# Kernel optimization log

Hardware: AMD Instinct MI355X
Metric: run time of the kernel (lower is better)

Reference implementation:

```python
import jax, jax.numpy as jnp
import numpy as np

B, N, H = 16, 1024, 768
NEG_INF = -9e15
SLOPE = 0.2


def setup_inputs() -> dict:
    key = jax.random.key(0)
    k1, k2, k3, k4, k5 = jax.random.split(key, 5)
    x = jax.random.normal(k1, (B, N, H), dtype=jnp.float32)
    # node_length acts as a per-node validity mask (float, used via outer product)
    lengths = jax.random.randint(k2, (B,), N // 2, N)
    node_length = (jnp.arange(N)[None, :] < lengths[:, None]).astype(jnp.float32)
    # sparse-ish binary adjacency with self-loops
    adj = (jax.random.uniform(k3, (B, N, N)) < 0.05).astype(jnp.float32)
    adj = jnp.maximum(adj, jnp.eye(N, dtype=jnp.float32)[None])
    # params: kaiming-normal init
    W = jax.random.normal(k4, (H, H), dtype=jnp.float32) * np.sqrt(2.0 / H)
    a = jax.random.normal(k5, (2 * H, 1), dtype=jnp.float32) * np.sqrt(2.0 / (2 * H))
    return {"input": x, "node_length": node_length, "graph_structure": adj, "W": W, "a": a}


def reference(input, node_length, graph_structure, W, a):
    # node_vec = A @ X  [B,N,H]
    node_vec = jnp.matmul(graph_structure, input)
    h = jnp.matmul(node_vec, W)  # [B,N,F]
    F_ = W.shape[1]
    a1 = a[:F_, 0]   # weights on h_i
    a2 = a[F_:, 0]   # weights on h_j
    # e[b,i,j] = leaky_relu(h_i . a1 + h_j . a2)  (identical to concat+matmul with a)
    s1 = jnp.einsum("bnf,f->bn", h, a1)
    s2 = jnp.einsum("bnf,f->bn", h, a2)
    e = jax.nn.leaky_relu(s1[:, :, None] + s2[:, None, :], negative_slope=SLOPE)
    # bias = outer product of node_length; mask where adj or bias <= 1e-6
    bias = node_length[:, :, None] * node_length[:, None, :]
    valid = (graph_structure > 1e-6) & (bias > 1e-6)
    scores = jnp.where(valid, e, NEG_INF)
    attn = jax.nn.softmax(scores, axis=-1)  # attn_dropout=0 -> identity
    return node_vec, attn
```

## Files before the change

kernel.cpp:

```cpp
#include <hip/hip_runtime.h>
#include <hip/hip_bf16.h>

#define BB 16
#define NN 1024
#define HH 768
#define NEG_INF_ -9.0e15f
#define SLOPE_ 0.2f

typedef __bf16 bh8 __attribute__((ext_vector_type(8)));
typedef __bf16 bh4 __attribute__((ext_vector_type(4)));
typedef float f4 __attribute__((ext_vector_type(4)));
typedef unsigned int u32;
typedef unsigned long long u64;


__device__ __forceinline__ float wave_sum0(float v) {
    #pragma unroll
    for (int off = 32; off > 0; off >>= 1) v += __shfl_down(v, off, 64);
    return v;
}
__device__ __forceinline__ float wave_sum_all(float v) {
    #pragma unroll
    for (int off = 1; off < 64; off <<= 1) v += __shfl_xor(v, off, 64);
    return v;
}
__device__ __forceinline__ float wave_max_all(float v) {
    #pragma unroll
    for (int off = 1; off < 64; off <<= 1) v = fmaxf(v, __shfl_xor(v, off, 64));
    return v;
}


__device__ __forceinline__ void gl_lds16(const void* g, void* l) {
    __builtin_amdgcn_global_load_lds(
        (const __attribute__((address_space(1))) u32*)g,
        (__attribute__((address_space(3))) u32*)l, 16, 0, 0);
}


__global__ __launch_bounds__(256) void prep_kernel(const float* __restrict__ adj,
                                                   const float* __restrict__ W,
                                                   const float* __restrict__ a,
                                                   u64* __restrict__ bits,
                                                   float* __restrict__ wa1,
                                                   float* __restrict__ wa2,
                                                   float* __restrict__ s1,
                                                   float* __restrict__ s2) {
    const int bid = blockIdx.x;
    const int tid = threadIdx.x;
    const int wave = tid >> 6, lane = tid & 63;

    const int gid = bid * 256 + tid;
    if (gid < BB * NN) { s1[gid] = 0.f; s2[gid] = 0.f; }

    const int row = bid * 4 + wave;
    const float* ar = adj + (size_t)row * NN;
    const int seg = lane >> 4;
    const int sh = (lane & 15) * 4;
    #pragma unroll
    for (int i = 0; i < 4; i++) {
        const int j = lane * 4 + i * 256;
        const float4 av = *(const float4*)(ar + j);
        u32 nib = (av.x > 1e-6f ? 1u : 0u) | (av.y > 1e-6f ? 2u : 0u)
                | (av.z > 1e-6f ? 4u : 0u) | (av.w > 1e-6f ? 8u : 0u);
        u64 word = (u64)nib << sh;
        word |= __shfl_xor(word, 8, 16);
        word |= __shfl_xor(word, 4, 16);
        word |= __shfl_xor(word, 2, 16);
        word |= __shfl_xor(word, 1, 16);
        if ((lane & 15) == 0) bits[(size_t)row * 16 + i * 4 + seg] = word;
    }

    if (bid < 192) {
        const int f = bid * 4 + wave;
        const float* Wr = W + (size_t)f * HH;
        float v1 = 0.f, v2 = 0.f;
        #pragma unroll
        for (int i = 0; i < 3; i++) {
            const int h = lane * 4 + i * 256;
            const float4 w  = *(const float4*)(Wr + h);
            const float4 a1 = *(const float4*)(a + h);
            const float4 a2 = *(const float4*)(a + HH + h);
            v1 += w.x * a1.x + w.y * a1.y + w.z * a1.z + w.w * a1.w;
            v2 += w.x * a2.x + w.y * a2.y + w.z * a2.z + w.w * a2.w;
        }
        v1 = wave_sum0(v1);
        v2 = wave_sum0(v2);
        if (lane == 0) { wa1[f] = v1; wa2[f] = v2; }
    }
}


__global__ __launch_bounds__(256) void xt_kernel(const float* __restrict__ x,
                                                 __bf16* __restrict__ xT) {
    __shared__ __bf16 T[32][36];
    const int b = blockIdx.z, nt = blockIdx.y, ht = blockIdx.x;
    const int t = threadIdx.x;
    const int r = t >> 3;
    const int c = (t & 7) * 4;
    const float4 v = *(const float4*)(x + ((size_t)b * NN + nt * 32 + r) * HH + ht * 32 + c);
    T[r][c + 0] = (__bf16)v.x; T[r][c + 1] = (__bf16)v.y;
    T[r][c + 2] = (__bf16)v.z; T[r][c + 3] = (__bf16)v.w;

    __syncthreads();
    const int h = t >> 3;
    const int nc = (t & 7) * 4;
    bh4 o = { T[nc + 0][h], T[nc + 1][h], T[nc + 2][h], T[nc + 3][h] };
    *(bh4*)(xT + ((size_t)b * HH + ht * 32 + h) * NN + nt * 32 + nc) = o;
}


#define BW 17

__global__ __launch_bounds__(256) void gemm_bits(const u64* __restrict__ bits,
                                                 const __bf16* __restrict__ xT,
                                                 const float* __restrict__ wa1,
                                                 const float* __restrict__ wa2,
                                                 float* __restrict__ out,
                                                 float* __restrict__ s1,
                                                 float* __restrict__ s2) {
    __shared__ __bf16 LUT[256 * 8];
    __shared__ u64 bitsL[128 * BW];
    __shared__ __bf16 Bs[128 * 64];
    const int b = blockIdx.z, bm = blockIdx.y, bn = blockIdx.x;
    const int tid = threadIdx.x, lane = tid & 63, wave = tid >> 6;
    const int wr = (wave >> 1) << 6;
    const int wc = (wave & 1) << 6;
    const int quad = lane >> 4, l16 = lane & 15;

    {
        bh8 e;
        #pragma unroll
        for (int j = 0; j < 8; j++) e[j] = ((tid >> j) & 1) ? (__bf16)1.0f : (__bf16)0.0f;
        *(bh8*)&LUT[tid * 8] = e;
    }
    {
        const u64* bg = bits + ((size_t)b * NN + bm * 128) * 16;
        #pragma unroll
        for (int q = 0; q < 8; q++) {
            const int g = tid * 8 + q;
            bitsL[(g >> 4) * BW + (g & 15)] = bg[g];
        }
    }

    const __bf16* Xb = xT + ((size_t)b * HH + bn * 128) * NN;

    f4 acc[4][4];
    #pragma unroll
    for (int i = 0; i < 4; i++)
        #pragma unroll
        for (int j = 0; j < 4; j++)
            acc[i][j] = (f4){0.f, 0.f, 0.f, 0.f};

    __syncthreads();

    for (int kt = 0; kt < NN; kt += 64) {
        #pragma unroll
        for (int it = 0; it < 4; it++) {
            const int c = tid + 256 * it;
            const int r = c >> 3, j = c & 7, kc = j ^ (r & 7);
            gl_lds16(Xb + (size_t)r * NN + kt + kc * 8, &Bs[r * 64 + j * 8]);
        }
        __syncthreads();

        const int w = kt >> 6;
        u64 aw[4];
        #pragma unroll
        for (int i = 0; i < 4; i++)
            aw[i] = bitsL[(wr + i * 16 + l16) * BW + w];

        #pragma unroll
        for (int s = 0; s < 2; s++) {
            bh8 af[4], bf_[4];
            #pragma unroll
            for (int i = 0; i < 4; i++) {
                const u32 byte = (u32)(aw[i] >> ((s * 4 + quad) * 8)) & 0xffu;
                af[i] = *(const bh8*)&LUT[byte * 8];
            }
            #pragma unroll
            for (int j = 0; j < 4; j++) {
                const int row = wc + j * 16 + l16;
                const int jj = (s * 4 + quad) ^ (row & 7);
                bf_[j] = *(const bh8*)&Bs[row * 64 + jj * 8];
            }
            #pragma unroll
            for (int i = 0; i < 4; i++)
                #pragma unroll
                for (int j = 0; j < 4; j++)
                    acc[i][j] = __builtin_amdgcn_mfma_f32_16x16x32_bf16(af[i], bf_[j], acc[i][j], 0, 0, 0);
        }
        __syncthreads();
    }

    float* Cb = out + (size_t)b * NN * HH + (size_t)bm * 128 * HH + bn * 128;
    const int rbase = wr + quad * 4;
    const int cbase = wc + l16;
    #pragma unroll
    for (int i = 0; i < 4; i++)
        #pragma unroll
        for (int j = 0; j < 4; j++)
            #pragma unroll
            for (int r = 0; r < 4; r++)
                Cb[(size_t)(rbase + i * 16 + r) * HH + cbase + j * 16] = acc[i][j][r];

    float w1j[4], w2j[4];
    #pragma unroll
    for (int j = 0; j < 4; j++) {
        w1j[j] = wa1[bn * 128 + cbase + j * 16];
        w2j[j] = wa2[bn * 128 + cbase + j * 16];
    }
    #pragma unroll
    for (int i = 0; i < 4; i++)
        #pragma unroll
        for (int r = 0; r < 4; r++) {
            float p1 = acc[i][0][r] * w1j[0] + acc[i][1][r] * w1j[1]
                     + acc[i][2][r] * w1j[2] + acc[i][3][r] * w1j[3];
            float p2 = acc[i][0][r] * w2j[0] + acc[i][1][r] * w2j[1]
                     + acc[i][2][r] * w2j[2] + acc[i][3][r] * w2j[3];
            p1 += __shfl_down(p1, 8, 16); p1 += __shfl_down(p1, 4, 16);
            p1 += __shfl_down(p1, 2, 16); p1 += __shfl_down(p1, 1, 16);
            p2 += __shfl_down(p2, 8, 16); p2 += __shfl_down(p2, 4, 16);
            p2 += __shfl_down(p2, 2, 16); p2 += __shfl_down(p2, 1, 16);
            if (l16 == 0) {
                const int n = b * NN + bm * 128 + rbase + i * 16 + r;
                atomicAdd(&s1[n], p1);
                atomicAdd(&s2[n], p2);
            }
        }
}


__global__ __launch_bounds__(256) void softmax_kernel(const u64* __restrict__ bits,
                                                      const float* __restrict__ nl,
                                                      const float* __restrict__ s1,
                                                      const float* __restrict__ s2,
                                                      float* __restrict__ attn) {
    const int row = blockIdx.x * 4 + (threadIdx.x >> 6);
    const int lane = threadIdx.x & 63;
    const int b = row >> 10, n = row & (NN - 1);
    const u64* bwr = bits + (size_t)row * 16;
    const float* nlb = nl + (size_t)b * NN;
    const float* s2b = s2 + (size_t)b * NN;
    const float s1v = s1[row];
    const bool rowok = nlb[n] > 1e-6f;
    const int bitbase = (lane & 15) * 4;

    f4 sc[4];
    float mx = NEG_INF_;
    #pragma unroll
    for (int i = 0; i < 4; i++) {
        const int j = lane * 4 + i * 256;
        const float4 sv = *(const float4*)(s2b + j);
        const float4 nv = *(const float4*)(nlb + j);
        const u64 w64 = bwr[i * 4 + (lane >> 4)];
        const float zs[4] = { s1v + sv.x, s1v + sv.y, s1v + sv.z, s1v + sv.w };
        const float ns[4] = { nv.x, nv.y, nv.z, nv.w };
        #pragma unroll
        for (int e = 0; e < 4; e++) {
            const float z = zs[e];
            const float lr = z > 0.f ? z : SLOPE_ * z;
            const bool valid = rowok && ((w64 >> (bitbase + e)) & 1ull) && (ns[e] > 1e-6f);
            sc[i][e] = valid ? lr : NEG_INF_;
            mx = fmaxf(mx, sc[i][e]);
        }
    }
    mx = wave_max_all(mx);

    f4 ex[4];
    float sum = 0.f;
    #pragma unroll
    for (int i = 0; i < 4; i++)
        #pragma unroll
        for (int e = 0; e < 4; e++) {
            ex[i][e] = __expf(sc[i][e] - mx);
            sum += ex[i][e];
        }
    sum = wave_sum_all(sum);
    const float inv = 1.0f / sum;

    float* outr = attn + (size_t)row * NN;
    #pragma unroll
    for (int i = 0; i < 4; i++) {
        const int j = lane * 4 + i * 256;
        float4 o;
        o.x = ex[i][0] * inv; o.y = ex[i][1] * inv;
        o.z = ex[i][2] * inv; o.w = ex[i][3] * inv;
        *(float4*)(outr + j) = o;
    }
}


extern "C" void kernel_launch(void* const* d_in, const int* in_sizes, int n_in,
                              void* d_out, int out_size, void* d_ws, size_t ws_size,
                              hipStream_t stream) {
    const float* x   = (const float*)d_in[0];
    const float* nl  = (const float*)d_in[1];
    const float* adj = (const float*)d_in[2];
    const float* W   = (const float*)d_in[3];
    const float* a   = (const float*)d_in[4];

    float* out = (float*)d_out;
    float* node_vec = out;
    float* attn = out + (size_t)BB * NN * HH;

    char* wsb = (char*)d_ws;
    float* wa1 = (float*)(wsb);
    float* wa2 = wa1 + HH;
    float* s1  = wa2 + HH;
    float* s2  = s1 + BB * NN;
    u64*    bits = (u64*)(wsb + (1u << 20));
    __bf16* xT   = (__bf16*)(wsb + (4u << 20));

    hipLaunchKernelGGL(prep_kernel, dim3(4096), dim3(256), 0, stream, adj, W, a, bits, wa1, wa2, s1, s2);
    hipLaunchKernelGGL(xt_kernel, dim3(24, 32, BB), dim3(256), 0, stream, x, xT);
    hipLaunchKernelGGL(gemm_bits, dim3(6, 8, BB), dim3(256), 0, stream, bits, xT, wa1, wa2, node_vec, s1, s2);
    hipLaunchKernelGGL(softmax_kernel, dim3(4096), dim3(256), 0, stream, bits, nl, s1, s2, attn);
}
```

Before: 275.2 us.

## Merge prep and transpose kernels, replace bitmask LUT A-tiles with dense bf16 adjacency

The adjacency prep and x-transpose kernels are merged into one launch using a split block index. The prep step now also writes a dense bf16 copy of the adjacency matrix. The GEMM streams that copy into LDS with async global-to-LDS loads, replacing the bitmask plus lookup-table decode of A fragments. This drops one launch and the LUT/bitmask LDS reads, but adds a 32 MB bf16 adjacency write in prep and 32 MB extra reads per GEMM pass instead of compact bits.

```diff
diff --git a/kernel.cpp b/kernel.cpp
--- a/kernel.cpp
+++ b/kernel.cpp
@@ -38,89 +38,92 @@
 }
 
 
-__global__ __launch_bounds__(256) void prep_kernel(const float* __restrict__ adj,
-                                                   const float* __restrict__ W,
-                                                   const float* __restrict__ a,
-                                                   u64* __restrict__ bits,
-                                                   float* __restrict__ wa1,
-                                                   float* __restrict__ wa2,
-                                                   float* __restrict__ s1,
-                                                   float* __restrict__ s2) {
+__global__ __launch_bounds__(256) void prep_xt_kernel(const float* __restrict__ adj,
+                                                      const float* __restrict__ W,
+                                                      const float* __restrict__ a,
+                                                      const float* __restrict__ x,
+                                                      u64* __restrict__ bits,
+                                                      __bf16* __restrict__ adjb,
+                                                      __bf16* __restrict__ xT,
+                                                      float* __restrict__ wa1,
+                                                      float* __restrict__ wa2,
+                                                      float* __restrict__ s1,
+                                                      float* __restrict__ s2) {
+    __shared__ __bf16 T[32][36];
     const int bid = blockIdx.x;
     const int tid = threadIdx.x;
     const int wave = tid >> 6, lane = tid & 63;
 
-    const int gid = bid * 256 + tid;
-    if (gid < BB * NN) { s1[gid] = 0.f; s2[gid] = 0.f; }
-
-    const int row = bid * 4 + wave;
-    const float* ar = adj + (size_t)row * NN;
-    const int seg = lane >> 4;
-    const int sh = (lane & 15) * 4;
-    #pragma unroll
-    for (int i = 0; i < 4; i++) {
-        const int j = lane * 4 + i * 256;
-        const float4 av = *(const float4*)(ar + j);
-        u32 nib = (av.x > 1e-6f ? 1u : 0u) | (av.y > 1e-6f ? 2u : 0u)
-                | (av.z > 1e-6f ? 4u : 0u) | (av.w > 1e-6f ? 8u : 0u);
-        u64 word = (u64)nib << sh;
-        word |= __shfl_xor(word, 8, 16);
-        word |= __shfl_xor(word, 4, 16);
-        word |= __shfl_xor(word, 2, 16);
-        word |= __shfl_xor(word, 1, 16);
-        if ((lane & 15) == 0) bits[(size_t)row * 16 + i * 4 + seg] = word;
-    }
-
-    if (bid < 192) {
-        const int f = bid * 4 + wave;
-        const float* Wr = W + (size_t)f * HH;
-        float v1 = 0.f, v2 = 0.f;
-        #pragma unroll
-        for (int i = 0; i < 3; i++) {
-            const int h = lane * 4 + i * 256;
-            const float4 w  = *(const float4*)(Wr + h);
-            const float4 a1 = *(const float4*)(a + h);
-            const float4 a2 = *(const float4*)(a + HH + h);
-            v1 += w.x * a1.x + w.y * a1.y + w.z * a1.z + w.w * a1.w;
-            v2 += w.x * a2.x + w.y * a2.y + w.z * a2.z + w.w * a2.w;
-        }
-        v1 = wave_sum0(v1);
-        v2 = wave_sum0(v2);
-        if (lane == 0) { wa1[f] = v1; wa2[f] = v2; }
-    }
-}
-
-
-__global__ __launch_bounds__(256) void xt_kernel(const float* __restrict__ x,
-                                                 __bf16* __restrict__ xT) {
-    __shared__ __bf16 T[32][36];
-    const int b = blockIdx.z, nt = blockIdx.y, ht = blockIdx.x;
-    const int t = threadIdx.x;
-    const int r = t >> 3;
-    const int c = (t & 7) * 4;
-    const float4 v = *(const float4*)(x + ((size_t)b * NN + nt * 32 + r) * HH + ht * 32 + c);
-    T[r][c + 0] = (__bf16)v.x; T[r][c + 1] = (__bf16)v.y;
-    T[r][c + 2] = (__bf16)v.z; T[r][c + 3] = (__bf16)v.w;
-
-    __syncthreads();
-    const int h = t >> 3;
-    const int nc = (t & 7) * 4;
-    bh4 o = { T[nc + 0][h], T[nc + 1][h], T[nc + 2][h], T[nc + 3][h] };
-    *(bh4*)(xT + ((size_t)b * HH + ht * 32 + h) * NN + nt * 32 + nc) = o;
-}
-
-
-#define BW 17
-
-__global__ __launch_bounds__(256) void gemm_bits(const u64* __restrict__ bits,
-                                                 const __bf16* __restrict__ xT,
-                                                 const float* __restrict__ wa1,
-                                                 const float* __restrict__ wa2,
-                                                 float* __restrict__ out,
-                                                 float* __restrict__ s1,
-                                                 float* __restrict__ s2) {
-    __shared__ __bf16 LUT[256 * 8];
-    __shared__ u64 bitsL[128 * BW];
+    if (bid < 4096) {
+        const int gid = bid * 256 + tid;
+        if (gid < BB * NN) { s1[gid] = 0.f; s2[gid] = 0.f; }
+
+        const int row = bid * 4 + wave;
+        const float* ar = adj + (size_t)row * NN;
+        __bf16* abr = adjb + (size_t)row * NN;
+        const int seg = lane >> 4;
+        const int sh = (lane & 15) * 4;
+        #pragma unroll
+        for (int i = 0; i < 4; i++) {
+            const int j = lane * 4 + i * 256;
+            const float4 av = *(const float4*)(ar + j);
+            bh4 o = { (__bf16)av.x, (__bf16)av.y, (__bf16)av.z, (__bf16)av.w };
+            *(bh4*)(abr + j) = o;
+            u32 nib = (av.x > 1e-6f ? 1u : 0u) | (av.y > 1e-6f ? 2u : 0u)
+                    | (av.z > 1e-6f ? 4u : 0u) | (av.w > 1e-6f ? 8u : 0u);
+            u64 word = (u64)nib << sh;
+            word |= __shfl_xor(word, 8, 16);
+            word |= __shfl_xor(word, 4, 16);
+            word |= __shfl_xor(word, 2, 16);
+            word |= __shfl_xor(word, 1, 16);
+            if ((lane & 15) == 0) bits[(size_t)row * 16 + i * 4 + seg] = word;
+        }
+
+        if (bid < 192) {
+            const int f = bid * 4 + wave;
+            const float* Wr = W + (size_t)f * HH;
+            float v1 = 0.f, v2 = 0.f;
+            #pragma unroll
+            for (int i = 0; i < 3; i++) {
+                const int h = lane * 4 + i * 256;
+                const float4 w  = *(const float4*)(Wr + h);
+                const float4 a1 = *(const float4*)(a + h);
+                const float4 a2 = *(const float4*)(a + HH + h);
+                v1 += w.x * a1.x + w.y * a1.y + w.z * a1.z + w.w * a1.w;
+                v2 += w.x * a2.x + w.y * a2.y + w.z * a2.z + w.w * a2.w;
+            }
+            v1 = wave_sum0(v1);
+            v2 = wave_sum0(v2);
+            if (lane == 0) { wa1[f] = v1; wa2[f] = v2; }
+        }
+    } else {
+        const int u = bid - 4096;
+        const int ht = u % 24;
+        const int nt = (u / 24) & 31;
+        const int b  = u / (24 * 32);
+        const int r = tid >> 3;
+        const int c = (tid & 7) * 4;
+        const float4 v = *(const float4*)(x + ((size_t)b * NN + nt * 32 + r) * HH + ht * 32 + c);
+        T[r][c + 0] = (__bf16)v.x; T[r][c + 1] = (__bf16)v.y;
+        T[r][c + 2] = (__bf16)v.z; T[r][c + 3] = (__bf16)v.w;
+
+        __syncthreads();
+        const int h = tid >> 3;
+        const int nc = (tid & 7) * 4;
+        bh4 o = { T[nc + 0][h], T[nc + 1][h], T[nc + 2][h], T[nc + 3][h] };
+        *(bh4*)(xT + ((size_t)b * HH + ht * 32 + h) * NN + nt * 32 + nc) = o;
+    }
+}
+
+
+__global__ __launch_bounds__(256) void gemm_dense(const __bf16* __restrict__ adjb,
+                                                  const __bf16* __restrict__ xT,
+                                                  const float* __restrict__ wa1,
+                                                  const float* __restrict__ wa2,
+                                                  float* __restrict__ out,
+                                                  float* __restrict__ s1,
+                                                  float* __restrict__ s2) {
+    __shared__ __bf16 As[128 * 64];
     __shared__ __bf16 Bs[128 * 64];
     const int b = blockIdx.z, bm = blockIdx.y, bn = blockIdx.x;
     const int tid = threadIdx.x, lane = tid & 63, wave = tid >> 6;
@@ -128,22 +131,18 @@
     const int wc = (wave & 1) << 6;
     const int quad = lane >> 4, l16 = lane & 15;
 
-    {
-        bh8 e;
-        #pragma unroll
-        for (int j = 0; j < 8; j++) e[j] = ((tid >> j) & 1) ? (__bf16)1.0f : (__bf16)0.0f;
-        *(bh8*)&LUT[tid * 8] = e;
-    }
-    {
-        const u64* bg = bits + ((size_t)b * NN + bm * 128) * 16;
-        #pragma unroll
-        for (int q = 0; q < 8; q++) {
-            const int g = tid * 8 + q;
-            bitsL[(g >> 4) * BW + (g & 15)] = bg[g];
-        }
-    }
-
-    const __bf16* Xb = xT + ((size_t)b * HH + bn * 128) * NN;
+    const __bf16* Ab = adjb + ((size_t)b * NN + bm * 128) * NN;
+    const __bf16* Xb = xT   + ((size_t)b * HH + bn * 128) * NN;
+
+    const __bf16* aSrc[4]; const __bf16* bSrc[4]; int dOff[4];
+    #pragma unroll
+    for (int it = 0; it < 4; it++) {
+        const int c = tid + 256 * it;
+        const int r = c >> 3, j = c & 7, kc = j ^ (r & 7);
+        aSrc[it] = Ab + (size_t)r * NN + kc * 8;
+        bSrc[it] = Xb + (size_t)r * NN + kc * 8;
+        dOff[it] = c * 8;
+    }
 
     f4 acc[4][4];
     #pragma unroll
@@ -152,30 +151,22 @@
         for (int j = 0; j < 4; j++)
             acc[i][j] = (f4){0.f, 0.f, 0.f, 0.f};
 
-    __syncthreads();
-
     for (int kt = 0; kt < NN; kt += 64) {
         #pragma unroll
         for (int it = 0; it < 4; it++) {
-            const int c = tid + 256 * it;
-            const int r = c >> 3, j = c & 7, kc = j ^ (r & 7);
-            gl_lds16(Xb + (size_t)r * NN + kt + kc * 8, &Bs[r * 64 + j * 8]);
+            gl_lds16(aSrc[it] + kt, &As[dOff[it]]);
+            gl_lds16(bSrc[it] + kt, &Bs[dOff[it]]);
         }
         __syncthreads();
-
-        const int w = kt >> 6;
-        u64 aw[4];
-        #pragma unroll
-        for (int i = 0; i < 4; i++)
-            aw[i] = bitsL[(wr + i * 16 + l16) * BW + w];
 
         #pragma unroll
         for (int s = 0; s < 2; s++) {
             bh8 af[4], bf_[4];
             #pragma unroll
             for (int i = 0; i < 4; i++) {
-                const u32 byte = (u32)(aw[i] >> ((s * 4 + quad) * 8)) & 0xffu;
-                af[i] = *(const bh8*)&LUT[byte * 8];
+                const int row = wr + i * 16 + l16;
+                const int jj = (s * 4 + quad) ^ (row & 7);
+                af[i] = *(const bh8*)&As[row * 64 + jj * 8];
             }
             #pragma unroll
             for (int j = 0; j < 4; j++) {
@@ -310,9 +301,11 @@
     float* s2  = s1 + BB * NN;
     u64*    bits = (u64*)(wsb + (1u << 20));
     __bf16* xT   = (__bf16*)(wsb + (4u << 20));
-
-    hipLaunchKernelGGL(prep_kernel, dim3(4096), dim3(256), 0, stream, adj, W, a, bits, wa1, wa2, s1, s2);
-    hipLaunchKernelGGL(xt_kernel, dim3(24, 32, BB), dim3(256), 0, stream, x, xT);
-    hipLaunchKernelGGL(gemm_bits, dim3(6, 8, BB), dim3(256), 0, stream, bits, xT, wa1, wa2, node_vec, s1, s2);
+    __bf16* adjb = (__bf16*)(wsb + (32u << 20));
+
+    hipLaunchKernelGGL(prep_xt_kernel, dim3(4096 + 24 * 32 * BB), dim3(256), 0, stream,
+                       adj, W, a, x, bits, adjb, xT, wa1, wa2, s1, s2);
+    hipLaunchKernelGGL(gemm_dense, dim3(6, 8, BB), dim3(256), 0, stream,
+                       adjb, xT, wa1, wa2, node_vec, s1, s2);
     hipLaunchKernelGGL(softmax_kernel, dim3(4096), dim3(256), 0, stream, bits, nl, s1, s2, attn);
 }
```

Result: slower. 285.6 us (+3.8%).
